# Performance work log

Measured on AMD Instinct MI355X. Metric: run time of the kernel, lower is better.

Reference implementation:

```python
import jax, jax.numpy as jnp
import numpy as np

B, H, W = 8, 64, 64
EMBED, HEADS, HEAD_DIM = 768, 12, 64
FF = 3072
WS = 14  # window size
SCALE = HEAD_DIM ** -0.5
EPS = 1e-6


def setup_inputs() -> dict:
    key = jax.random.key(0)
    ks = jax.random.split(key, 8)
    def n(k, shp, s=0.02):
        return jax.random.normal(k, shp, jnp.float32) * s
    return {
        "x": jax.random.normal(ks[0], (B, H, W, EMBED), jnp.float32),
        "g1": jnp.ones((EMBED,), jnp.float32),
        "beta1": jnp.zeros((EMBED,), jnp.float32),
        "w_qkv": n(ks[1], (EMBED, 3 * EMBED)),
        "b_qkv": jnp.zeros((3 * EMBED,), jnp.float32),
        "w_proj": n(ks[2], (EMBED, EMBED)),
        "b_proj": jnp.zeros((EMBED,), jnp.float32),
        "rel_pos_h": n(ks[3], (2 * WS - 1, HEAD_DIM)),
        "rel_pos_w": n(ks[4], (2 * WS - 1, HEAD_DIM)),
        "g2": jnp.ones((EMBED,), jnp.float32),
        "beta2": jnp.zeros((EMBED,), jnp.float32),
        "w_fc1": n(ks[5], (EMBED, FF)),
        "b_fc1": jnp.zeros((FF,), jnp.float32),
        "w_fc2": n(ks[6], (FF, EMBED)),
        "b_fc2": jnp.zeros((EMBED,), jnp.float32),
    }


def layer_norm(x, g, b):
    m = jnp.mean(x, axis=-1, keepdims=True)
    v = jnp.mean(jnp.square(x - m), axis=-1, keepdims=True)
    return (x - m) * jax.lax.rsqrt(v + EPS) * g + b


def window_partition(x):
    b, h, w, c = x.shape
    ph, pw = (-h) % WS, (-w) % WS
    x = jnp.pad(x, ((0, 0), (0, ph), (0, pw), (0, 0)))
    hp, wp = h + ph, w + pw
    x = x.reshape(b, hp // WS, WS, wp // WS, WS, c)
    x = x.transpose(0, 1, 3, 2, 4, 5).reshape(-1, WS, WS, c)
    return x, (hp, wp)


def window_unpartition(win, pad_hw, hw):
    hp, wp = pad_hw
    h, w = hw
    b = win.shape[0] // ((hp // WS) * (wp // WS))
    x = win.reshape(b, hp // WS, wp // WS, WS, WS, -1)
    x = x.transpose(0, 1, 3, 2, 4, 5).reshape(b, hp, wp, -1)
    return x[:, :h, :w, :]


def attention(xw, w_qkv, b_qkv, w_proj, b_proj, rel_pos_h, rel_pos_w):
    bw, hs, ws_, c = xw.shape
    n = hs * ws_
    qkv = (xw.reshape(bw, n, c) @ w_qkv + b_qkv).reshape(bw, n, 3, HEADS, HEAD_DIM)
    q, k, v = jnp.moveaxis(qkv, 2, 0)            # each (bw, n, heads, hd)
    q = q.transpose(0, 2, 1, 3)                  # (bw, heads, n, hd)
    k = k.transpose(0, 2, 1, 3)
    v = v.transpose(0, 2, 1, 3)
    attn = jnp.einsum('bhnd,bhmd->bhnm', q * SCALE, k)
    # decomposed relative position bias (q unscaled, per torch reference)
    idx = jnp.arange(WS)[:, None] - jnp.arange(WS)[None, :] + (WS - 1)
    Rh = rel_pos_h[idx]                          # (ws, ws, hd)
    Rw = rel_pos_w[idx]
    r_q = q.reshape(bw, HEADS, WS, WS, HEAD_DIM)
    rel_h = jnp.einsum('bhpqd,pkd->bhpqk', r_q, Rh)
    rel_w = jnp.einsum('bhpqd,qkd->bhpqk', r_q, Rw)
    attn = attn.reshape(bw, HEADS, WS, WS, WS, WS)
    attn = attn + rel_h[..., :, None] + rel_w[..., None, :]
    attn = jax.nn.softmax(attn.reshape(bw, HEADS, n, n), axis=-1)
    out = jnp.einsum('bhnm,bhmd->bhnd', attn, v)
    out = out.transpose(0, 2, 1, 3).reshape(bw, hs, ws_, c)
    return out @ w_proj + b_proj


def reference(x, g1, beta1, w_qkv, b_qkv, w_proj, b_proj, rel_pos_h, rel_pos_w,
              g2, beta2, w_fc1, b_fc1, w_fc2, b_fc2):
    shortcut = x
    h = layer_norm(x, g1, beta1)
    win, pad_hw = window_partition(h)
    a = attention(win, w_qkv, b_qkv, w_proj, b_proj, rel_pos_h, rel_pos_w)
    a = window_unpartition(a, pad_hw, (x.shape[1], x.shape[2]))
    x = shortcut + a
    h2 = layer_norm(x, g2, beta2)
    mlp = jax.nn.gelu(h2 @ w_fc1 + b_fc1, approximate=False) @ w_fc2 + b_fc2
    return x + mlp
```

## Files before the change

### kernel.cpp

```cpp
#include <hip/hip_runtime.h>
#include <cstdint>


typedef unsigned short u16;
typedef __attribute__((ext_vector_type(8))) short short8;
typedef __attribute__((ext_vector_type(4))) float f32x4;

__device__ __forceinline__ u16 f2b(float f) {
    union { float f; unsigned int i; } x; x.f = f;
    unsigned int u = x.i;
    return (u16)((u + 0x7fffu + ((u >> 16) & 1u)) >> 16);
}
__device__ __forceinline__ float b2f(u16 u) {
    union { unsigned int i; float f; } x; x.i = ((unsigned int)u) << 16; return x.f;
}

__device__ __forceinline__ void gload16(const u16* g, u16* l) {
    __builtin_amdgcn_global_load_lds(
        (const __attribute__((address_space(1))) unsigned int*)g,
        (__attribute__((address_space(3))) unsigned int*)l, 16, 0, 0);
}

__device__ __forceinline__ int xcd_swz(int bid, int nwg) {
    int q = nwg >> 3, r = nwg & 7;
    int x = bid & 7, lo = bid >> 3;
    return (x < r ? x * (q + 1) : r * (q + 1) + (x - r) * q) + lo;
}

__global__ __launch_bounds__(256) void transpose_k(
    const float* __restrict__ in, u16* __restrict__ out, int R, int C)
{
    __shared__ float tile[32][33];
    int bpc = C >> 5;
    int r0 = (blockIdx.x / bpc) << 5;
    int c0 = (blockIdx.x % bpc) << 5;
    int lx = threadIdx.x & 31, ly = threadIdx.x >> 5;
#pragma unroll
    for (int s = 0; s < 32; s += 8)
        tile[ly + s][lx] = in[(size_t)(r0 + ly + s) * C + c0 + lx];
    __syncthreads();
#pragma unroll
    for (int s = 0; s < 32; s += 8)
        out[(size_t)(c0 + ly + s) * R + r0 + lx] = f2b(tile[lx][ly + s]);
}

__global__ __launch_bounds__(256) void ln_kernel(
    const float* __restrict__ in, const float* __restrict__ g,
    const float* __restrict__ beta, u16* __restrict__ out, int windowed,
    int row_base)
{
    __shared__ float sbuf[4];
    int tid = threadIdx.x;
    size_t orow = (size_t)blockIdx.x * 768;
    size_t irow;
    if (windowed) {
        int r = row_base + blockIdx.x;
        int win = r / 196, t = r % 196;
        int p = t / 14, q = t % 14;
        int b = win / 25, wt = win % 25;
        int i = (wt / 5) * 14 + p, j = (wt % 5) * 14 + q;
        if (i >= 64 || j >= 64) {
            out[orow + tid] = 0; out[orow + tid + 256] = 0; out[orow + tid + 512] = 0;
            return;
        }
        irow = (((size_t)b * 64 + i) * 64 + j) * 768;
    } else {
        irow = (size_t)blockIdx.x * 768;
    }
    float v0 = in[irow + tid];
    float v1 = in[irow + tid + 256];
    float v2 = in[irow + tid + 512];
    float s = v0 + v1 + v2;
#pragma unroll
    for (int off = 32; off; off >>= 1) s += __shfl_xor(s, off, 64);
    if ((tid & 63) == 0) sbuf[tid >> 6] = s;
    __syncthreads();
    float mean = (sbuf[0] + sbuf[1] + sbuf[2] + sbuf[3]) * (1.f / 768.f);
    __syncthreads();
    float d0 = v0 - mean, d1 = v1 - mean, d2 = v2 - mean;
    float sq = d0 * d0 + d1 * d1 + d2 * d2;
#pragma unroll
    for (int off = 32; off; off >>= 1) sq += __shfl_xor(sq, off, 64);
    if ((tid & 63) == 0) sbuf[tid >> 6] = sq;
    __syncthreads();
    float var = (sbuf[0] + sbuf[1] + sbuf[2] + sbuf[3]) * (1.f / 768.f);
    float rs = rsqrtf(var + 1e-6f);
    out[orow + tid]       = f2b(d0 * rs * g[tid]       + beta[tid]);
    out[orow + tid + 256] = f2b(d1 * rs * g[tid + 256] + beta[tid + 256]);
    out[orow + tid + 512] = f2b(d2 * rs * g[tid + 512] + beta[tid + 512]);
}


__device__ __forceinline__ short8 lds_frag256(const u16* base, int row, int ks,
                                              int quad) {
    return *(const short8*)(base + row * 64 + ((((ks << 2) + quad) ^ (row & 7)) << 3));
}

__device__ __forceinline__ void compute_tile256(
    const u16* Ab, const u16* Bb, f32x4 (&acc)[8][4],
    int wr, int wc, int quad, int l16)
{
    short8 b_[4][2];
#pragma unroll
    for (int n = 0; n < 4; n++)
#pragma unroll
        for (int ks = 0; ks < 2; ks++)
            b_[n][ks] = lds_frag256(Bb, wc * 64 + n * 16 + l16, ks, quad);
#pragma unroll
    for (int mq = 0; mq < 2; mq++) {
        short8 a_[4][2];
#pragma unroll
        for (int m = 0; m < 4; m++)
#pragma unroll
            for (int ks = 0; ks < 2; ks++)
                a_[m][ks] = lds_frag256(Ab, wr * 128 + mq * 64 + m * 16 + l16, ks, quad);
        __builtin_amdgcn_s_setprio(1);
#pragma unroll
        for (int m = 0; m < 4; m++)
#pragma unroll
            for (int n = 0; n < 4; n++)
#pragma unroll
                for (int ks = 0; ks < 2; ks++)
                    acc[mq * 4 + m][n] = __builtin_amdgcn_mfma_f32_16x16x32_bf16(
                        a_[m][ks], b_[n][ks], acc[mq * 4 + m][n], 0, 0, 0);
        __builtin_amdgcn_s_setprio(0);
    }
}

template <int EPI>
__global__ __launch_bounds__(512) void gemm256(
    const u16* __restrict__ A, const u16* __restrict__ Bt,
    const float* __restrict__ bias, void* __restrict__ CoutV,
    const float* __restrict__ resid, int M, int N, int K, int row_base)
{
    __shared__ __align__(16) u16 As0[256 * 64];
    __shared__ __align__(16) u16 As1[256 * 64];
    __shared__ __align__(16) u16 Bs0[256 * 64];
    __shared__ __align__(16) u16 Bs1[256 * 64];

    const int tid = threadIdx.x;
    const int lane = tid & 63, wave = tid >> 6;
    const int wr = wave >> 2, wc = wave & 3;
    const int quad = lane >> 4, l16 = lane & 15;
    const int ntile = N / 256;
    const int swz = xcd_swz(blockIdx.x, gridDim.x);
    const int m0 = (swz / ntile) * 256;
    const int n0 = (swz % ntile) * 256;

    const int rl = lane >> 3;
    const int cl = ((lane & 7) ^ rl) << 3;
    int aoff[4], boff[4];
#pragma unroll
    for (int q = 0; q < 4; q++) {
        aoff[q] = (m0 + wave * 32 + q * 8 + rl) * K + cl;
        boff[q] = (n0 + wave * 32 + q * 8 + rl) * K + cl;
    }
    const int lws = wave * 2048;

    f32x4 acc[8][4] = {};
    const int nth = K >> 7;

#pragma unroll
    for (int q = 0; q < 4; q++) {
        gload16(A  + aoff[q], As0 + lws + q * 512);
        gload16(Bt + boff[q], Bs0 + lws + q * 512);
    }

#pragma unroll 1
    for (int it = 0; it < nth; ++it) {
        __builtin_amdgcn_sched_barrier(0);
        __builtin_amdgcn_s_barrier();
        __builtin_amdgcn_sched_barrier(0);
        {
            const int k1 = (2 * it + 1) << 6;
#pragma unroll
            for (int q = 0; q < 4; q++) {
                gload16(A  + aoff[q] + k1, As1 + lws + q * 512);
                gload16(Bt + boff[q] + k1, Bs1 + lws + q * 512);
            }
        }
        __builtin_amdgcn_sched_barrier(0);
        asm volatile("s_waitcnt vmcnt(8)" ::: "memory");
        __builtin_amdgcn_sched_barrier(0);
        __builtin_amdgcn_s_barrier();
        __builtin_amdgcn_sched_barrier(0);
        compute_tile256(As0, Bs0, acc, wr, wc, quad, l16);

        __builtin_amdgcn_sched_barrier(0);
        __builtin_amdgcn_s_barrier();
        __builtin_amdgcn_sched_barrier(0);
        if (it + 1 < nth) {
            const int k2 = (2 * it + 2) << 6;
#pragma unroll
            for (int q = 0; q < 4; q++) {
                gload16(A  + aoff[q] + k2, As0 + lws + q * 512);
                gload16(Bt + boff[q] + k2, Bs0 + lws + q * 512);
            }
            __builtin_amdgcn_sched_barrier(0);
            asm volatile("s_waitcnt vmcnt(8)" ::: "memory");
        } else {
            __builtin_amdgcn_sched_barrier(0);
            asm volatile("s_waitcnt vmcnt(0)" ::: "memory");
        }
        __builtin_amdgcn_sched_barrier(0);
        __builtin_amdgcn_s_barrier();
        __builtin_amdgcn_sched_barrier(0);
        compute_tile256(As1, Bs1, acc, wr, wc, quad, l16);
    }

#pragma unroll
    for (int mi = 0; mi < 8; mi++) {
#pragma unroll
        for (int ni = 0; ni < 4; ni++) {
            const int gn = n0 + wc * 64 + ni * 16 + l16;
            const float bv = bias[gn];
#pragma unroll
            for (int r = 0; r < 4; r++) {
                const int row = m0 + wr * 128 + mi * 16 + quad * 4 + r;
                if (row >= M) continue;
                float v = acc[mi][ni][r] + bv;
                if (EPI == 0) {
                    ((u16*)CoutV)[(size_t)row * N + gn] = f2b(v);
                } else if (EPI == 1) {
                    int grow = row_base + row;
                    int win = grow / 196, t = grow % 196;
                    int p = t / 14, q = t % 14;
                    int b_ = win / 25, wt = win % 25;
                    int i = (wt / 5) * 14 + p, j = (wt % 5) * 14 + q;
                    if (i < 64 && j < 64) {
                        size_t idx = (((size_t)b_ * 64 + i) * 64 + j) * 768 + gn;
                        ((float*)CoutV)[idx] = resid[idx] + v;
                    }
                } else if (EPI == 2) {
                    float gl = 0.5f * v * (1.0f + erff(v * 0.70710678118654752f));
                    ((u16*)CoutV)[(size_t)row * N + gn] = f2b(gl);
                } else {
                    size_t idx = (size_t)(row_base + row) * 768 + gn;
                    ((float*)CoutV)[idx] = resid[idx] + v;
                }
            }
        }
    }
}

#define AT_W 72
#define PB_W 40

__global__ __launch_bounds__(256) void attn_mfma(
    const u16* __restrict__ qkv,
    const float* __restrict__ relh, const float* __restrict__ relw,
    u16* __restrict__ out)
{
    __shared__ __align__(16) u16 pbuf[4][32 * PB_W];
    __shared__ __align__(16) u16 Kc[64 * AT_W];
    __shared__ __align__(16) u16 Vt[64 * AT_W];
    u16* rel_ext = &pbuf[0][0];

    const int nwg = gridDim.x;
    const int swzb = xcd_swz(blockIdx.x, nwg);
    const int win = swzb / 24, rem = swzb % 24;
    const int head = rem >> 1, half = rem & 1;
    const int row0 = half * 128;
    const int tid = threadIdx.x, lane = tid & 63, wave = tid >> 6;
    const int quad = lane >> 4, l16 = lane & 15;
    const size_t base = (size_t)win * 196 * 2304 + (size_t)head * 64;

    short8 qf[2][2];
#pragma unroll
    for (int mi = 0; mi < 2; mi++) {
        int tok = row0 + wave * 32 + mi * 16 + l16;
        int rt = tok < 196 ? tok : 195;
        const u16* qp = qkv + base + (size_t)rt * 2304 + quad * 8;
        qf[mi][0] = *(const short8*)(qp);
        qf[mi][1] = *(const short8*)(qp + 32);
    }

    for (int e = tid; e < 64 * 64; e += 256) {
        int rr = e >> 6, cc = e & 63;
        float v = 0.f;
        if (rr < 27)      v = 8.f * relh[rr * 64 + cc];
        else if (rr < 54) v = 8.f * relw[(rr - 27) * 64 + cc];
        Kc[rr * AT_W + cc] = f2b(v);
    }
    if (tid < 128) {
        u16* rp = rel_ext + tid * 32;
        uint4 z = make_uint4(0u, 0u, 0u, 0u);
        *(uint4*)(rp) = z; *(uint4*)(rp + 8) = z;
        *(uint4*)(rp + 16) = z; *(uint4*)(rp + 24) = z;
        rp[31] = f2b(-1e30f);
    }
    __syncthreads();

#pragma unroll
    for (int cb = 0; cb < 2; cb++) {
#pragma unroll
        for (int nt = 0; nt < 2; nt++) {
            const u16* kp_ = Kc + (cb * 32 + nt * 16 + l16) * AT_W + quad * 8;
            short8 b0 = *(const short8*)(kp_);
            short8 b1 = *(const short8*)(kp_ + 32);
            int i = cb * 32 + nt * 16 + l16;
#pragma unroll
            for (int mi = 0; mi < 2; mi++) {
                f32x4 c = {};
                c = __builtin_amdgcn_mfma_f32_16x16x32_bf16(qf[mi][0], b0, c, 0, 0, 0);
                c = __builtin_amdgcn_mfma_f32_16x16x32_bf16(qf[mi][1], b1, c, 0, 0, 0);
#pragma unroll
                for (int r = 0; r < 4; r++) {
                    int row = wave * 32 + mi * 16 + quad * 4 + r;
                    int grow = row0 + row;
                    int rowB = grow < 196 ? grow : 195;
                    int p = rowB / 14, qq = rowB % 14;
                    if (i < 27) {
                        int t = p + 13 - i;
                        if (t >= 0 && t < 14) rel_ext[row * 32 + t] = f2b(c[r]);
                    } else if (i < 54) {
                        int t = qq + 13 - (i - 27);
                        if (t >= 0 && t < 14) rel_ext[row * 32 + 14 + t] = f2b(c[r]);
                    }
                }
            }
        }
    }
    short8 qe[2];
#pragma unroll
    for (int mi = 0; mi < 2; mi++)
        qe[mi] = *(const short8*)(rel_ext + (wave * 32 + mi * 16 + l16) * 32 + quad * 8);

    f32x4 acc[2][4] = {};
    float ml_[2][4], ll_[2][4];
#pragma unroll
    for (int mi = 0; mi < 2; mi++)
#pragma unroll
        for (int r = 0; r < 4; r++) { ml_[mi][r] = -1e30f; ll_[mi][r] = 0.f; }

#pragma unroll 1
    for (int c = 0; c < 4; c++) {
        const int kbase = c * 64;
        __syncthreads();
        {
            int key = tid >> 2;
            int cg  = (tid & 3) << 4;
            int gk = kbase + key;
            uint4 k0 = make_uint4(0u,0u,0u,0u), k1 = k0, v0 = k0, v1 = k0;
            if (gk < 196) {
                const u16* kp_ = qkv + base + 768  + (size_t)gk * 2304 + cg;
                const u16* vp_ = qkv + base + 1536 + (size_t)gk * 2304 + cg;
                k0 = *(const uint4*)(kp_); k1 = *(const uint4*)(kp_ + 8);
                v0 = *(const uint4*)(vp_); v1 = *(const uint4*)(vp_ + 8);
            }
            *(uint4*)(Kc + key * AT_W + cg)     = k0;
            *(uint4*)(Kc + key * AT_W + cg + 8) = k1;
            union { uint4 u; u16 h[8]; } a, b; a.u = v0; b.u = v1;
#pragma unroll
            for (int i = 0; i < 8; i++) Vt[(cg + i) * AT_W + key] = a.h[i];
#pragma unroll
            for (int i = 0; i < 8; i++) Vt[(cg + 8 + i) * AT_W + key] = b.h[i];
        }
        __syncthreads();

        short8 bo[4];
        {
            const u16 one = 0x3F80;
#pragma unroll
            for (int nt = 0; nt < 4; nt++) {
                int key = kbase + nt * 16 + l16;
                int inval = key >= 196;
                int kp = key / 14, kq = key - kp * 14;
                union { short8 s; u16 h[8]; } u;
#pragma unroll
                for (int j = 0; j < 8; j++) {
                    int t = quad * 8 + j;
                    u16 v = 0;
                    if (!inval && t == kp) v = one;
                    if (!inval && t >= 14 && (t - 14) == kq) v = one;
                    if (inval && t == 31) v = one;
                    u.h[j] = v;
                }
                bo[nt] = u.s;
            }
        }

        f32x4 s23[2][2];
#pragma unroll
        for (int mi = 0; mi < 2; mi++) {
            f32x4 s[4];
            __builtin_amdgcn_s_setprio(1);
#pragma unroll
            for (int nt = 0; nt < 4; nt++) {
                const u16* kp_ = Kc + (nt * 16 + l16) * AT_W + quad * 8;
                short8 kf0 = *(const short8*)(kp_);
                short8 kf1 = *(const short8*)(kp_ + 32);
                f32x4 t = {};
                t = __builtin_amdgcn_mfma_f32_16x16x32_bf16(qf[mi][0], kf0, t, 0, 0, 0);
                t = __builtin_amdgcn_mfma_f32_16x16x32_bf16(qf[mi][1], kf1, t, 0, 0, 0);
                t = __builtin_amdgcn_mfma_f32_16x16x32_bf16(qe[mi],    bo[nt], t, 0, 0, 0);
                s[nt] = t * 0.125f;
            }
            __builtin_amdgcn_s_setprio(0);
#pragma unroll
            for (int r = 0; r < 4; r++) {
                float mx = fmaxf(fmaxf(s[0][r], s[1][r]), fmaxf(s[2][r], s[3][r]));
#pragma unroll
                for (int off = 8; off; off >>= 1) mx = fmaxf(mx, __shfl_xor(mx, off, 16));
                float mo = ml_[mi][r];
                float mn = fmaxf(mo, mx);
                float alpha = __expf(mo - mn);
                ml_[mi][r] = mn;
                float p0 = __expf(s[0][r] - mn), p1 = __expf(s[1][r] - mn);
                float p2 = __expf(s[2][r] - mn), p3 = __expf(s[3][r] - mn);
                float ps = (p0 + p1) + (p2 + p3);
#pragma unroll
                for (int off = 8; off; off >>= 1) ps += __shfl_xor(ps, off, 16);
                ll_[mi][r] = ll_[mi][r] * alpha + ps;
#pragma unroll
                for (int ni = 0; ni < 4; ni++) acc[mi][ni][r] *= alpha;
                s[0][r] = p0; s[1][r] = p1; s[2][r] = p2; s[3][r] = p3;
            }
#pragma unroll
            for (int nt = 0; nt < 2; nt++)
#pragma unroll
                for (int r = 0; r < 4; r++)
                    pbuf[wave][(mi * 16 + quad * 4 + r) * PB_W + nt * 16 + l16] = f2b(s[nt][r]);
            s23[mi][0] = s[2]; s23[mi][1] = s[3];
        }

        __builtin_amdgcn_s_setprio(1);
#pragma unroll
        for (int mi = 0; mi < 2; mi++) {
            short8 pf = *(const short8*)(pbuf[wave] + (mi * 16 + l16) * PB_W + quad * 8);
#pragma unroll
            for (int ni = 0; ni < 4; ni++) {
                short8 vfn = *(const short8*)(Vt + (ni * 16 + l16) * AT_W + quad * 8);
                acc[mi][ni] = __builtin_amdgcn_mfma_f32_16x16x32_bf16(pf, vfn, acc[mi][ni], 0, 0, 0);
            }
        }
        __builtin_amdgcn_s_setprio(0);
#pragma unroll
        for (int mi = 0; mi < 2; mi++)
#pragma unroll
            for (int h = 0; h < 2; h++)
#pragma unroll
                for (int r = 0; r < 4; r++)
                    pbuf[wave][(mi * 16 + quad * 4 + r) * PB_W + h * 16 + l16] = f2b(s23[mi][h][r]);
        __builtin_amdgcn_s_setprio(1);
#pragma unroll
        for (int mi = 0; mi < 2; mi++) {
            short8 pf = *(const short8*)(pbuf[wave] + (mi * 16 + l16) * PB_W + quad * 8);
#pragma unroll
            for (int ni = 0; ni < 4; ni++) {
                short8 vfn = *(const short8*)(Vt + (ni * 16 + l16) * AT_W + 32 + quad * 8);
                acc[mi][ni] = __builtin_amdgcn_mfma_f32_16x16x32_bf16(pf, vfn, acc[mi][ni], 0, 0, 0);
            }
        }
        __builtin_amdgcn_s_setprio(0);
    }

#pragma unroll
    for (int mi = 0; mi < 2; mi++)
#pragma unroll
        for (int r = 0; r < 4; r++) {
            int tok = row0 + wave * 32 + mi * 16 + quad * 4 + r;
            if (tok < 196) {
                float inv = 1.f / ll_[mi][r];
                size_t ob = (size_t)(win * 196 + tok) * 768 + head * 64;
#pragma unroll
                for (int ni = 0; ni < 4; ni++)
                    out[ob + ni * 16 + l16] = f2b(acc[mi][ni][r] * inv);
            }
        }
}

extern "C" void kernel_launch(void* const* d_in, const int* in_sizes, int n_in,
                              void* d_out, int out_size, void* d_ws, size_t ws_size,
                              hipStream_t stream)
{
    const float* x      = (const float*)d_in[0];
    const float* g1     = (const float*)d_in[1];
    const float* beta1  = (const float*)d_in[2];
    const float* w_qkv  = (const float*)d_in[3];
    const float* b_qkv  = (const float*)d_in[4];
    const float* w_proj = (const float*)d_in[5];
    const float* b_proj = (const float*)d_in[6];
    const float* rph    = (const float*)d_in[7];
    const float* rpw    = (const float*)d_in[8];
    const float* g2     = (const float*)d_in[9];
    const float* beta2  = (const float*)d_in[10];
    const float* w_fc1  = (const float*)d_in[11];
    const float* b_fc1  = (const float*)d_in[12];
    const float* w_fc2  = (const float*)d_in[13];
    const float* b_fc2  = (const float*)d_in[14];
    float* out = (float*)d_out;

    const size_t WT = 14155776;
    size_t b1 = 0, b2 = 0;
    int nc = 0, mc = 0;
    auto fits = [&](int a, int m) -> bool {
        size_t rows = (size_t)(200 / a) * 196, toks = (size_t)32768 / m;
        size_t bb1 = rows * 768 * 2 >= toks * 768 * 2 ? rows * 768 * 2 : toks * 768 * 2;
        size_t bb2 = rows * 2304 * 2 >= toks * 3072 * 2 ? rows * 2304 * 2 : toks * 3072 * 2;
        if (WT + bb1 + bb2 <= ws_size) { b1 = bb1; b2 = bb2; nc = a; mc = m; return true; }
        return false;
    };
    if (!fits(1, 1) && !fits(1, 2) && !fits(2, 2) && !fits(2, 4) && !fits(4, 4))
        return;

    char* ws = (char*)d_ws;
    u16* wt0 = (u16*)ws;
    u16* wt1 = wt0 + 2304 * 768;
    u16* wt2 = wt1 + 768 * 768;
    u16* wt3 = wt2 + 3072 * 768;
    u16* buf1 = (u16*)(ws + WT);
    u16* buf2 = (u16*)(ws + WT + b1);

    dim3 blk(256), blk5(512);

    transpose_k<<<(768/32)*(2304/32), blk, 0, stream>>>(w_qkv,  wt0, 768, 2304);
    transpose_k<<<(768/32)*(768/32),  blk, 0, stream>>>(w_proj, wt1, 768, 768);
    transpose_k<<<(768/32)*(3072/32), blk, 0, stream>>>(w_fc1,  wt2, 768, 3072);
    transpose_k<<<(3072/32)*(768/32), blk, 0, stream>>>(w_fc2,  wt3, 3072, 768);

    {
        const int nw = 200 / nc, rows = nw * 196;
        const int mt = (rows + 255) / 256;
        for (int c = 0; c < nc; c++) {
            const int rb = c * rows;
            ln_kernel<<<rows, blk, 0, stream>>>(x, g1, beta1, buf1, 1, rb);
            gemm256<0><<<dim3(mt * (2304/256)), blk5, 0, stream>>>(
                buf1, wt0, b_qkv, buf2, nullptr, rows, 2304, 768, 0);
            attn_mfma<<<nw * 24, blk, 0, stream>>>(buf2, rph, rpw, buf1);
            gemm256<1><<<dim3(mt * (768/256)), blk5, 0, stream>>>(
                buf1, wt1, b_proj, out, x, rows, 768, 768, rb);
        }
    }

    {
        const int tk = 32768 / mc;
        const int mt2 = (tk + 255) / 256;
        for (int c = 0; c < mc; c++) {
            const int rb = c * tk;
            ln_kernel<<<tk, blk, 0, stream>>>(
                out + (size_t)rb * 768, g2, beta2, buf1, 0, 0);
            gemm256<2><<<dim3(mt2 * (3072/256)), blk5, 0, stream>>>(
                buf1, wt2, b_fc1, buf2, nullptr, tk, 3072, 768, 0);
            gemm256<3><<<dim3(mt2 * (768/256)), blk5, 0, stream>>>(
                buf2, wt3, b_fc2, out, out, tk, 768, 3072, rb);
        }
    }
}
```

Before: 1.560 ms.

## Deepen GEMM pipeline to four-stage K32 LDS buffering with new swizzle

Replaces the two-stage 64-wide K double buffer in the 256x256 GEMM with a four-stage ring of 32-wide K slices, keeping three tiles of global loads in flight. It also uses a new LDS swizzle suited to 32-element rows and interleaves fragment loads with MFMA groups. The goal is to hide global load latency better at the same LDS footprint, at the cost of twice as many barriers per unit of K and smaller MFMA bursts between them. The unrolled-by-four loop assumes K/32 is a multiple of four.

```diff
diff --git a/kernel.cpp b/kernel.cpp
--- a/kernel.cpp
+++ b/kernel.cpp
@@ -91,41 +91,86 @@
 }
 
 
-__device__ __forceinline__ short8 lds_frag256(const u16* base, int row, int ks,
-                                              int quad) {
-    return *(const short8*)(base + row * 64 + ((((ks << 2) + quad) ^ (row & 7)) << 3));
-}
-
-__device__ __forceinline__ void compute_tile256(
-    const u16* Ab, const u16* Bb, f32x4 (&acc)[8][4],
-    int wr, int wc, int quad, int l16)
+__device__ __forceinline__ short8 ldsf(const u16* P, int r, int quad) {
+    return *(const short8*)(P + r * 32 + ((quad ^ ((r >> 1) & 3)) << 3));
+}
+
+__device__ __forceinline__ void comp32(const u16* __restrict__ Ap,
+                                       const u16* __restrict__ Bp,
+                                       f32x4 (&acc)[8][4],
+                                       int wr, int wc, int quad, int l16)
 {
-    short8 b_[4][2];
-#pragma unroll
-    for (int n = 0; n < 4; n++)
-#pragma unroll
-        for (int ks = 0; ks < 2; ks++)
-            b_[n][ks] = lds_frag256(Bb, wc * 64 + n * 16 + l16, ks, quad);
-#pragma unroll
-    for (int mq = 0; mq < 2; mq++) {
-        short8 a_[4][2];
-#pragma unroll
-        for (int m = 0; m < 4; m++)
-#pragma unroll
-            for (int ks = 0; ks < 2; ks++)
-                a_[m][ks] = lds_frag256(Ab, wr * 128 + mq * 64 + m * 16 + l16, ks, quad);
-        __builtin_amdgcn_s_setprio(1);
-#pragma unroll
-        for (int m = 0; m < 4; m++)
-#pragma unroll
-            for (int n = 0; n < 4; n++)
-#pragma unroll
-                for (int ks = 0; ks < 2; ks++)
-                    acc[mq * 4 + m][n] = __builtin_amdgcn_mfma_f32_16x16x32_bf16(
-                        a_[m][ks], b_[n][ks], acc[mq * 4 + m][n], 0, 0, 0);
-        __builtin_amdgcn_s_setprio(0);
-    }
-}
+    short8 a[4], b[4];
+#pragma unroll
+    for (int n = 0; n < 2; n++) b[n] = ldsf(Bp, wc * 64 + n * 16 + l16, quad);
+#pragma unroll
+    for (int m = 0; m < 4; m++) a[m] = ldsf(Ap, wr * 128 + m * 16 + l16, quad);
+    __builtin_amdgcn_s_setprio(1);
+#pragma unroll
+    for (int m = 0; m < 4; m++)
+#pragma unroll
+        for (int n = 0; n < 2; n++)
+            acc[m][n] = __builtin_amdgcn_mfma_f32_16x16x32_bf16(
+                a[m], b[n], acc[m][n], 0, 0, 0);
+    __builtin_amdgcn_s_setprio(0);
+#pragma unroll
+    for (int n = 0; n < 2; n++) b[2 + n] = ldsf(Bp, wc * 64 + (2 + n) * 16 + l16, quad);
+    __builtin_amdgcn_s_setprio(1);
+#pragma unroll
+    for (int m = 0; m < 4; m++)
+#pragma unroll
+        for (int n = 0; n < 2; n++)
+            acc[m][2 + n] = __builtin_amdgcn_mfma_f32_16x16x32_bf16(
+                a[m], b[2 + n], acc[m][2 + n], 0, 0, 0);
+    __builtin_amdgcn_s_setprio(0);
+#pragma unroll
+    for (int m = 0; m < 4; m++) a[m] = ldsf(Ap, wr * 128 + 64 + m * 16 + l16, quad);
+    __builtin_amdgcn_s_setprio(1);
+#pragma unroll
+    for (int m = 0; m < 4; m++)
+#pragma unroll
+        for (int n = 0; n < 2; n++)
+            acc[4 + m][2 + n] = __builtin_amdgcn_mfma_f32_16x16x32_bf16(
+                a[m], b[2 + n], acc[4 + m][2 + n], 0, 0, 0);
+    __builtin_amdgcn_s_setprio(0);
+    __builtin_amdgcn_s_setprio(1);
+#pragma unroll
+    for (int m = 0; m < 4; m++)
+#pragma unroll
+        for (int n = 0; n < 2; n++)
+            acc[4 + m][n] = __builtin_amdgcn_mfma_f32_16x16x32_bf16(
+                a[m], b[n], acc[4 + m][n], 0, 0, 0);
+    __builtin_amdgcn_s_setprio(0);
+}
+
+#define STAGE4(SA, SB, TT)                                                 \
+    if ((TT) < nt) {                                                       \
+        const size_t kk = (size_t)((TT) << 5);                             \
+        gload16(A  + aoff0 + kk, (SA) + wbase);                            \
+        gload16(A  + aoff1 + kk, (SA) + 4096 + wbase);                     \
+        gload16(Bt + boff0 + kk, (SB) + wbase);                            \
+        gload16(Bt + boff1 + kk, (SB) + 4096 + wbase);                     \
+    }
+
+#define GSTEP(CA, CB, SA, SB, TT)                                          \
+    {                                                                      \
+        __builtin_amdgcn_sched_barrier(0);                                 \
+        __builtin_amdgcn_s_barrier();    \
+        __builtin_amdgcn_sched_barrier(0);                                 \
+        STAGE4(SA, SB, (TT) + 3);                                          \
+        __builtin_amdgcn_sched_barrier(0);                                 \
+        {                                                                  \
+            const int d = nt - 1 - (TT);                                   \
+            if (d >= 3)      asm volatile("s_waitcnt vmcnt(12)" ::: "memory"); \
+            else if (d == 2) asm volatile("s_waitcnt vmcnt(8)"  ::: "memory"); \
+            else if (d == 1) asm volatile("s_waitcnt vmcnt(4)"  ::: "memory"); \
+            else             asm volatile("s_waitcnt vmcnt(0)"  ::: "memory"); \
+        }                                                                  \
+        __builtin_amdgcn_sched_barrier(0);                                 \
+        __builtin_amdgcn_s_barrier();    \
+        __builtin_amdgcn_sched_barrier(0);                                 \
+        comp32(CA, CB, acc, wr, wc, quad, l16);                            \
+    }
 
 template <int EPI>
 __global__ __launch_bounds__(512) void gemm256(
@@ -133,10 +178,14 @@
     const float* __restrict__ bias, void* __restrict__ CoutV,
     const float* __restrict__ resid, int M, int N, int K, int row_base)
 {
-    __shared__ __align__(16) u16 As0[256 * 64];
-    __shared__ __align__(16) u16 As1[256 * 64];
-    __shared__ __align__(16) u16 Bs0[256 * 64];
-    __shared__ __align__(16) u16 Bs1[256 * 64];
+    __shared__ __align__(16) u16 As0[256 * 32];
+    __shared__ __align__(16) u16 As1[256 * 32];
+    __shared__ __align__(16) u16 As2[256 * 32];
+    __shared__ __align__(16) u16 As3[256 * 32];
+    __shared__ __align__(16) u16 Bs0[256 * 32];
+    __shared__ __align__(16) u16 Bs1[256 * 32];
+    __shared__ __align__(16) u16 Bs2[256 * 32];
+    __shared__ __align__(16) u16 Bs3[256 * 32];
 
     const int tid = threadIdx.x;
     const int lane = tid & 63, wave = tid >> 6;
@@ -147,65 +196,27 @@
     const int m0 = (swz / ntile) * 256;
     const int n0 = (swz % ntile) * 256;
 
-    const int rl = lane >> 3;
-    const int cl = ((lane & 7) ^ rl) << 3;
-    int aoff[4], boff[4];
-#pragma unroll
-    for (int q = 0; q < 4; q++) {
-        aoff[q] = (m0 + wave * 32 + q * 8 + rl) * K + cl;
-        boff[q] = (n0 + wave * 32 + q * 8 + rl) * K + cl;
-    }
-    const int lws = wave * 2048;
+    const int rA   = (wave << 4) + (lane >> 2);
+    const int kcol = (((lane & 3) ^ ((rA >> 1) & 3)) << 3);
+    const size_t aoff0 = (size_t)(m0 + rA) * K + kcol;
+    const size_t aoff1 = aoff0 + (size_t)128 * K;
+    const size_t boff0 = (size_t)(n0 + rA) * K + kcol;
+    const size_t boff1 = boff0 + (size_t)128 * K;
+    const int wbase = wave * 512;
 
     f32x4 acc[8][4] = {};
-    const int nth = K >> 7;
-
-#pragma unroll
-    for (int q = 0; q < 4; q++) {
-        gload16(A  + aoff[q], As0 + lws + q * 512);
-        gload16(Bt + boff[q], Bs0 + lws + q * 512);
-    }
+    const int nt = K >> 5;
+
+    STAGE4(As0, Bs0, 0);
+    STAGE4(As1, Bs1, 1);
+    STAGE4(As2, Bs2, 2);
 
 #pragma unroll 1
-    for (int it = 0; it < nth; ++it) {
-        __builtin_amdgcn_sched_barrier(0);
-        __builtin_amdgcn_s_barrier();
-        __builtin_amdgcn_sched_barrier(0);
-        {
-            const int k1 = (2 * it + 1) << 6;
-#pragma unroll
-            for (int q = 0; q < 4; q++) {
-                gload16(A  + aoff[q] + k1, As1 + lws + q * 512);
-                gload16(Bt + boff[q] + k1, Bs1 + lws + q * 512);
-            }
-        }
-        __builtin_amdgcn_sched_barrier(0);
-        asm volatile("s_waitcnt vmcnt(8)" ::: "memory");
-        __builtin_amdgcn_sched_barrier(0);
-        __builtin_amdgcn_s_barrier();
-        __builtin_amdgcn_sched_barrier(0);
-        compute_tile256(As0, Bs0, acc, wr, wc, quad, l16);
-
-        __builtin_amdgcn_sched_barrier(0);
-        __builtin_amdgcn_s_barrier();
-        __builtin_amdgcn_sched_barrier(0);
-        if (it + 1 < nth) {
-            const int k2 = (2 * it + 2) << 6;
-#pragma unroll
-            for (int q = 0; q < 4; q++) {
-                gload16(A  + aoff[q] + k2, As0 + lws + q * 512);
-                gload16(Bt + boff[q] + k2, Bs0 + lws + q * 512);
-            }
-            __builtin_amdgcn_sched_barrier(0);
-            asm volatile("s_waitcnt vmcnt(8)" ::: "memory");
-        } else {
-            __builtin_amdgcn_sched_barrier(0);
-            asm volatile("s_waitcnt vmcnt(0)" ::: "memory");
-        }
-        __builtin_amdgcn_sched_barrier(0);
-        __builtin_amdgcn_s_barrier();
-        __builtin_amdgcn_sched_barrier(0);
-        compute_tile256(As1, Bs1, acc, wr, wc, quad, l16);
+    for (int t = 0; t < nt; t += 4) {
+        GSTEP(As0, Bs0, As3, Bs3, t);
+        GSTEP(As1, Bs1, As0, Bs0, t + 1);
+        GSTEP(As2, Bs2, As1, Bs1, t + 2);
+        GSTEP(As3, Bs3, As2, Bs2, t + 3);
     }
 
 #pragma unroll
```

After: 1.548 ms. Within noise of the previous version (-0.7%).
